# Optimization experiments

Hardware: AMD Instinct MI355X
Metric: run time of the kernel (lower is better)

Reference implementation:

```python
import jax, jax.numpy as jnp
import numpy as np

B, N, C = 16, 4096, 80
IOU_THR = 0.5
CONF_THR = 0.5
MAX_DET = 100
FROM_LOGITS = True


def setup_inputs() -> dict:
    key = jax.random.key(0)
    k1, k2 = jax.random.split(key)
    box_prediction = jax.random.uniform(k1, (B, N, 4), dtype=jnp.float32)
    class_prediction = jax.random.normal(k2, (B, N, C), dtype=jnp.float32)
    return {"box_prediction": box_prediction, "class_prediction": class_prediction}


def _pairwise_iou(b):
    # TF NMS kernel semantics: corners [y1,x1,y2,x2], normalized with min/max.
    y1 = jnp.minimum(b[:, 0], b[:, 2]); y2 = jnp.maximum(b[:, 0], b[:, 2])
    x1 = jnp.minimum(b[:, 1], b[:, 3]); x2 = jnp.maximum(b[:, 1], b[:, 3])
    area = (y2 - y1) * (x2 - x1)                      # [N]
    ih = jnp.maximum(0.0, jnp.minimum(y2[:, None], y2[None, :]) - jnp.maximum(y1[:, None], y1[None, :]))
    iw = jnp.maximum(0.0, jnp.minimum(x2[:, None], x2[None, :]) - jnp.maximum(x1[:, None], x1[None, :]))
    inter = ih * iw                                   # [N, N]
    union = area[:, None] + area[None, :] - inter
    return jnp.where(inter > 0.0, inter / union, 0.0)


def _nms_single(boxes, cls):
    # boxes [N,4], cls [N,C] -> padded ([MAX_DET,4], [MAX_DET,C])
    scores = jnp.max(cls, axis=1)                     # tf.reduce_max(cls_pred, axis=1)
    order = jnp.argsort(-scores)                      # descending, stable
    b = boxes[order]
    s = scores[order]
    valid = s > CONF_THR                              # score_threshold filter
    iou = _pairwise_iou(b)                            # [N, N]

    def body(keep, i):
        suppressed = jnp.any(keep & (iou[:, i] > IOU_THR))
        k = valid[i] & jnp.logical_not(suppressed)
        return keep.at[i].set(k), None

    keep, _ = jax.lax.scan(body, jnp.zeros(boxes.shape[0], dtype=bool), jnp.arange(boxes.shape[0]))
    # Compact kept boxes to the front (stable sort keeps descending-score order),
    # take the first MAX_DET slots, zero-pad the rest (fixed-shape analogue of
    # tf.image.non_max_suppression's variable-length index output).
    pos = jnp.argsort(jnp.logical_not(keep))[:MAX_DET]
    m = (jnp.arange(MAX_DET) < jnp.sum(keep))[:, None]
    out_idx = order[pos]
    nms_box = jnp.where(m, boxes[out_idx], 0.0)
    nms_cls = jnp.where(m, cls[out_idx], 0.0)
    return nms_box, nms_cls


def reference(box_prediction, class_prediction):
    # bounding_box_format == 'xywh' (absolute) -> convert_format is identity.
    if FROM_LOGITS:
        cls_predictions = jax.nn.softmax(jnp.square(class_prediction * 10.0), axis=-1)
    else:
        cls_predictions = class_prediction
    nms_box, nms_cls = jax.vmap(_nms_single)(box_prediction, cls_predictions)
    return nms_box, nms_cls, cls_predictions
```

## Files before the change

### kernel.cpp

```cpp
#include <hip/hip_runtime.h>
#include <cstdint>
#include <cstddef>

#define BB 16
#define NN 4096
#define CC 80
#define MAXD 100
#define CONF_T 0.5f
#define PER_B (MAXD * 4 + MAXD * CC)
#define NWORDS 64
#define FBCAP 2048
#define SEGSZ 2048

#define IOUC 0x1.000001p-1

#define WS_KEYS   0x000000
#define WS_NEED   0x200000

__global__ __launch_bounds__(256) void k_softmax(const float* __restrict__ cls_in,
                                                 float* __restrict__ probs,
                                                 uint64_t* __restrict__ keys) {
#pragma clang fp contract(off)
    int slot = blockIdx.x * 256 + threadIdx.x;
    int row  = slot >> 3;
    int j    = slot & 7;
    const float* rp = cls_in + (size_t)row * CC + j;

    float e[10];
    float m = -3.402823466e+38f;
    #pragma unroll
    for (int k = 0; k < 10; ++k) {
        float y = rp[8 * k] * 10.0f;
        float z = y * y;
        e[k] = z;
        m = fmaxf(m, z);
    }
    m = fmaxf(m, __shfl_xor(m, 1));
    m = fmaxf(m, __shfl_xor(m, 2));
    m = fmaxf(m, __shfl_xor(m, 4));

    #pragma unroll
    for (int k = 0; k < 10; ++k) e[k] = expf(e[k] - m);

    float acc = e[0];
    #pragma unroll
    for (int k = 1; k < 10; ++k) acc += e[k];
    acc = acc + __shfl_xor(acc, 1);
    acc = acc + __shfl_xor(acc, 2);
    acc = acc + __shfl_xor(acc, 4);

    float score = 1.0f / acc;
    float* pp = probs + (size_t)row * CC + j;
    #pragma unroll
    for (int k = 0; k < 10; ++k) pp[8 * k] = e[k] * score;

    if (j == 0) {
        unsigned n = (unsigned)(row & (NN - 1));
        keys[row] = ((uint64_t)__float_as_uint(score) << 32)
                  | (uint64_t)(0xFFFFFFFFu - n);
    }
}

__global__ __launch_bounds__(1024) void k_pnms(const uint64_t* __restrict__ keys,
                                               const float* __restrict__ boxes,
                                               const float* __restrict__ probs,
                                               float* __restrict__ out_box,
                                               float* __restrict__ out_cls) {
#pragma clang fp contract(off)
    __shared__ __align__(16) unsigned char sraw[6 * NN * 4];
    float* hy1 = (float*)sraw;
    float* hx1 = (float*)(sraw + NN * 4);
    float* hy2 = (float*)(sraw + 2 * NN * 4);
    float* hx2 = (float*)(sraw + 3 * NN * 4);
    float* har = (float*)(sraw + 4 * NN * 4);
    int*   og  = (int*)(sraw + 5 * NN * 4);
    uint64_t* bbuf = (uint64_t*)sraw;
    __shared__ uint64_t kill[64];
    __shared__ uint64_t persup[16];
    __shared__ float ky1[MAXD], kx1[MAXD], ky2[MAXD], kx2[MAXD], kar[MAXD];
    __shared__ int kpos[MAXD];
    __shared__ int fidx[MAXD];
    __shared__ int wsumA[16], wsumB[16];
    __shared__ int kept_s, done_s;

    const int tid = threadIdx.x, lane = tid & 63, wv = tid >> 6;
    const int b = blockIdx.x;
    const uint64_t* kb = keys + (size_t)b * NN;
    const float* bxp = boxes + (size_t)b * NN * 4;

    uint64_t myk[4]; bool fa[4], fb[4];
    int asum = 0, bsum = 0;
    for (int k = 0; k < 4; ++k) {
        uint64_t key = kb[4 * tid + k]; myk[k] = key;
        unsigned hi = (unsigned)(key >> 32);
        fa[k] = (hi == 0x3F800000u);
        fb[k] = (__uint_as_float(hi) > CONF_T) && !fa[k];
        asum += fa[k] ? 1 : 0; bsum += fb[k] ? 1 : 0;
    }
    int ia = asum, ib = bsum;
    for (int off = 1; off < 64; off <<= 1) {
        int va = __shfl_up(ia, off), vb = __shfl_up(ib, off);
        if (lane >= off) { ia += va; ib += vb; }
    }
    if (lane == 63) { wsumA[wv] = ia; wsumB[wv] = ib; }
    __syncthreads();
    int baseA = 0, baseB = 0, cntA = 0, cntB = 0;
    for (int w2 = 0; w2 < 16; ++w2) {
        if (w2 < wv) { baseA += wsumA[w2]; baseB += wsumB[w2]; }
        cntA += wsumA[w2]; cntB += wsumB[w2];
    }
    int pA = baseA + (ia - asum);
    int pB = baseB + (ib - bsum);
    for (int k = 0; k < 4; ++k) {
        if (fa[k]) og[pA++] = 4 * tid + k;
        if (fb[k]) bbuf[pB++] = myk[k];
    }
    __syncthreads();

    for (int i = tid; i < cntB; i += 1024) {
        uint64_t ki = bbuf[i];
        int rank = 0;
        for (int j = 0; j < cntB; ++j) rank += (bbuf[j] > ki) ? 1 : 0;
        og[cntA + rank] = (int)(0xFFFFFFFFu - (unsigned)(ki & 0xFFFFFFFFull));
    }
    int nl = cntA + cntB; if (nl > NN) nl = NN;
    __syncthreads();

    for (int i = tid; i < nl; i += 1024) {
        int o = og[i];
        float4 bv = ((const float4*)bxp)[o];
        float y1 = fminf(bv.x, bv.z), y2 = fmaxf(bv.x, bv.z);
        float x1 = fminf(bv.y, bv.w), x2 = fmaxf(bv.y, bv.w);
        hy1[i] = y1; hx1[i] = x1; hy2[i] = y2; hx2[i] = x2;
        har[i] = (y2 - y1) * (x2 - x1);
    }
    if (tid == 0) { kept_s = 0; done_s = 0; }

    int ng = (nl + 63) >> 6;
    for (int g = 0; g < ng; ++g) {
        __syncthreads();
        if (done_s) break;
        int kt = kept_s;
        int i = g * 64 + lane;
        bool v = i < nl;
        int ii = v ? i : 0;
        float y1 = hy1[ii], x1 = hx1[ii], y2 = hy2[ii], x2 = hx2[ii], ar = har[ii];

        bool killed = false;
        for (int q = wv; q < kt; q += 16) {
            float qy1 = ky1[q], qx1 = kx1[q], qy2 = ky2[q], qx2 = kx2[q], qar = kar[q];
            float ih = fmaxf(0.f, fminf(y2, qy2) - fmaxf(y1, qy1));
            float iw = fmaxf(0.f, fminf(x2, qx2) - fmaxf(x1, qx1));
            float inter = ih * iw;
            float uni = (ar + qar) - inter;
            killed = killed || (inter > 0.f && (double)inter > (double)uni * IOUC);
        }
        uint64_t pw = __ballot((!v) || killed);
        if (lane == 0) persup[wv] = pw;
        __syncthreads();
        uint64_t sup0 = 0;
        #pragma unroll
        for (int w2 = 0; w2 < 16; ++w2) sup0 |= persup[w2];
        if (sup0 == ~0ull) continue;

        #pragma unroll
        for (int r = 0; r < 4; ++r) {
            int t = wv + 16 * r;
            int it = g * 64 + t;
            bool tv = it < nl;
            int itx = tv ? it : 0;
            float ty1 = hy1[itx], tx1 = hx1[itx], ty2 = hy2[itx], tx2 = hx2[itx], tar = har[itx];
            float ih = fmaxf(0.f, fminf(ty2, y2) - fmaxf(ty1, y1));
            float iw = fmaxf(0.f, fminf(tx2, x2) - fmaxf(tx1, x1));
            float inter = ih * iw;
            float uni = (tar + ar) - inter;
            bool s = tv && v && (inter > 0.f) && ((double)inter > (double)uni * IOUC);
            uint64_t w = __ballot(s);
            if (lane == 0) kill[t] = w;
        }
        __syncthreads();

        if (wv == 0) {
            uint64_t sup = sup0, keptm = 0;
            #pragma unroll
            for (int c8 = 0; c8 < 8; ++c8) {
                uint64_t kk[8];
                #pragma unroll
                for (int u = 0; u < 8; ++u) kk[u] = kill[c8 * 8 + u];
                #pragma unroll
                for (int u = 0; u < 8; ++u) {
                    int t = c8 * 8 + u;
                    if (!((sup >> t) & 1ull)) { keptm |= 1ull << t; sup |= kk[u]; }
                }
            }
            int k0 = kept_s;
            if ((keptm >> lane) & 1ull) {
                int pos = k0 + __popcll(keptm & ((1ull << lane) - 1ull));
                if (pos < MAXD) {
                    kpos[pos] = i;
                    ky1[pos] = y1; kx1[pos] = x1;
                    ky2[pos] = y2; kx2[pos] = x2; kar[pos] = ar;
                }
            }
            if (lane == 0) {
                int k1 = k0 + __popcll(keptm);
                kept_s = k1;
                done_s = (k1 >= MAXD) ? 1 : 0;
            }
        }
    }
    __syncthreads();

    int kt = kept_s; if (kt > MAXD) kt = MAXD;
    if (tid < MAXD) fidx[tid] = (tid < kt) ? og[kpos[tid]] : 0;
    __syncthreads();

    float* ob = out_box + (size_t)b * MAXD * 4;
    float* oc = out_cls + (size_t)b * MAXD * CC;
    const float* pb = probs + (size_t)b * NN * CC;
    for (int r = tid; r < MAXD * 4; r += 1024) {
        int t = r >> 2, e2 = r & 3;
        float val = 0.0f;
        if (t < kt) { int idx = fidx[t]; val = bxp[(size_t)idx * 4 + e2]; }
        ob[r] = val;
    }
    for (int q = tid; q < MAXD * CC; q += 1024) {
        int t = q / CC, c = q - t * CC;
        float val = 0.0f;
        if (t < kt) { int idx = fidx[t]; val = pb[(size_t)idx * CC + c]; }
        oc[q] = val;
    }
}

__global__ __launch_bounds__(256) void k_gather(const float* __restrict__ boxes,
                                                const float* __restrict__ probs,
                                                const int* __restrict__ kidx,
                                                const int* __restrict__ cnt,
                                                float* __restrict__ out_box,
                                                float* __restrict__ out_cls) {
    int u = blockIdx.x * 256 + threadIdx.x;
    if (u >= BB * PER_B) return;
    int b = u / PER_B;
    int r = u - b * PER_B;
    int count = cnt[b];
    float val = 0.0f;
    if (r < MAXD * 4) {
        int t = r >> 2, e = r & 3;
        if (t < count) {
            int idx = kidx[b * MAXD + t];
            val = boxes[((size_t)b * NN + idx) * 4 + e];
        }
        out_box[(size_t)b * MAXD * 4 + r] = val;
    } else {
        int q = r - MAXD * 4;
        int t = q / CC, c = q - t * CC;
        if (t < count) {
            int idx = kidx[b * MAXD + t];
            val = probs[((size_t)b * NN + idx) * CC + c];
        }
        out_cls[(size_t)b * MAXD * CC + q] = val;
    }
}

__global__ __launch_bounds__(1024) void k_nms_fb(uint64_t* keys,
                                                 const float* __restrict__ boxes,
                                                 int* __restrict__ kidx_out,
                                                 int* __restrict__ cnt_out) {
#pragma clang fp contract(off)
    __shared__ float sy1[SEGSZ], sx1[SEGSZ], sy2[SEGSZ], sx2[SEGSZ];
    __shared__ int   soidx[SEGSZ];
    __shared__ uint64_t bbuf[FBCAP];
    __shared__ uint64_t sup[NWORDS];
    __shared__ float ky1[MAXD], kx1[MAXD], ky2[MAXD], kx2[MAXD], kar[MAXD];
    __shared__ int   keptidx[MAXD];
    __shared__ int   wsumA[16], wsumB[16];
    __shared__ int   keptcnt_s, ctrl_s, seg_s;

    const int tid = threadIdx.x, lane = tid & 63, wv = tid >> 6;
    const int b = blockIdx.x;
    const uint64_t* kb = keys + (size_t)b * NN;
    const float* bxp = boxes + (size_t)b * NN * 4;
    int* og = (int*)(keys + (size_t)b * NN);

    uint64_t myk[4]; bool fa[4], fb[4];
    int asum = 0, bsum = 0;
    for (int k = 0; k < 4; ++k) {
        uint64_t key = kb[4 * tid + k]; myk[k] = key;
        unsigned hi = (unsigned)(key >> 32);
        fa[k] = (hi == 0x3F800000u);
        fb[k] = (__uint_as_float(hi) > CONF_T) && !fa[k];
        asum += fa[k] ? 1 : 0; bsum += fb[k] ? 1 : 0;
    }
    int ia = asum, ib = bsum;
    for (int off = 1; off < 64; off <<= 1) {
        int va = __shfl_up(ia, off), vb = __shfl_up(ib, off);
        if (lane >= off) { ia += va; ib += vb; }
    }
    if (lane == 63) { wsumA[wv] = ia; wsumB[wv] = ib; }
    __syncthreads();
    int baseA = 0, baseB = 0, cntA = 0, cntB = 0;
    for (int w2 = 0; w2 < 16; ++w2) {
        if (w2 < wv) { baseA += wsumA[w2]; baseB += wsumB[w2]; }
        cntA += wsumA[w2]; cntB += wsumB[w2];
    }
    int pA = baseA + (ia - asum);
    int pB = baseB + (ib - bsum);
    for (int k = 0; k < 4; ++k) {
        if (fa[k]) og[pA++] = 4 * tid + k;
        if (fb[k]) { if (pB < FBCAP) bbuf[pB] = myk[k]; pB++; }
    }
    int cntBc = cntB < FBCAP ? cntB : FBCAP;
    int nlist = cntA + cntBc;
    if (tid == 0) { keptcnt_s = 0; seg_s = 0; }
    for (int i = tid; i < FBCAP; i += 1024) if (i >= cntB) bbuf[i] = 0;
    __syncthreads();

    for (unsigned k2 = 2; k2 <= FBCAP; k2 <<= 1) {
        for (unsigned j = k2 >> 1; j > 0; j >>= 1) {
            for (unsigned i = tid; i < FBCAP; i += 1024) {
                unsigned p = i ^ j;
                if (p > i) {
                    uint64_t va = bbuf[i], vb = bbuf[p];
                    bool desc = ((i & k2) == 0);
                    if (desc ? (va < vb) : (va > vb)) { bbuf[i] = vb; bbuf[p] = va; }
                }
            }
            __syncthreads();
        }
    }
    for (int i = tid; i < cntBc; i += 1024)
        og[cntA + i] = (int)(0xFFFFFFFFu - (unsigned)(bbuf[i] & 0xFFFFFFFFull));
    if (tid < NWORDS) {
        int lo = tid * 64;
        uint64_t mm;
        if (nlist <= lo) mm = ~0ull;
        else if (nlist >= lo + 64) mm = 0ull;
        else mm = (~0ull) << (nlist - lo);
        sup[tid] = mm;
    }
    __syncthreads();

    for (int i = tid; i < SEGSZ; i += 1024) {
        if (i < nlist) {
            int o = og[i];
            soidx[i] = o;
            const float* bp = bxp + (size_t)o * 4;
            float b0 = bp[0], b1 = bp[1], b2 = bp[2], b3 = bp[3];
            sy1[i] = fminf(b0, b2); sy2[i] = fmaxf(b0, b2);
            sx1[i] = fminf(b1, b3); sx2[i] = fmaxf(b1, b3);
        }
    }
    __syncthreads();

    int curw = 0, segr = 0;
    while (true) {
        if (tid == 0) {
            int code = -1;
            for (;;) {
                int wend = (segr + 1) * (SEGSZ / 64);
                if (curw >= wend) {
                    if (segr == 0 && nlist > SEGSZ) {
                        code = -2; segr = 1; seg_s = 1; curw = SEGSZ / 64;
                    } else code = -1;
                    break;
                }
                uint64_t live = ~sup[curw];
                if (live) {
                    int j = __ffsll((unsigned long long)live) - 1;
                    int sel = curw * 64 + j;
                    int li = sel - segr * SEGSZ;
                    int kc = keptcnt_s;
                    keptidx[kc] = soidx[li];
                    ky1[kc] = sy1[li]; kx1[kc] = sx1[li];
                    ky2[kc] = sy2[li]; kx2[kc] = sx2[li];
                    kar[kc] = (sy2[li] - sy1[li]) * (sx2[li] - sx1[li]);
                    keptcnt_s = kc + 1;
                    sup[curw] |= (1ull << j);
                    code = (kc + 1 >= MAXD) ? -1 : sel;
                    break;
                }
                ++curw;
            }
            ctrl_s = code;
        }
        __syncthreads();
        int c = ctrl_s;
        if (c == -1) break;

        if (c == -2) {
            for (int i = tid; i < SEGSZ; i += 1024) {
                int gi = SEGSZ + i;
                if (gi < nlist) {
                    int o = og[gi];
                    soidx[i] = o;
                    const float* bp = bxp + (size_t)o * 4;
                    float b0 = bp[0], b1 = bp[1], b2 = bp[2], b3 = bp[3];
                    sy1[i] = fminf(b0, b2); sy2[i] = fmaxf(b0, b2);
                    sx1[i] = fminf(b1, b3); sx2[i] = fmaxf(b1, b3);
                }
            }
            __syncthreads();
            int kc = keptcnt_s;
            for (int k = 0; k < 2; ++k) {
                int li = tid + k * 1024;
                float y1 = sy1[li], y2 = sy2[li], x1 = sx1[li], x2 = sx2[li];
                float ar = (y2 - y1) * (x2 - x1);
                bool s = false;
                for (int q = 0; q < kc; ++q) {
                    float ih = fmaxf(0.f, fminf(y2, ky2[q]) - fmaxf(y1, ky1[q]));
                    float iw = fmaxf(0.f, fminf(x2, kx2[q]) - fmaxf(x1, kx1[q]));
                    float inter = ih * iw;
                    float uni = (ar + kar[q]) - inter;
                    s = s || (inter > 0.f && inter / uni > 0.5f);
                }
                uint64_t bal = __ballot(s);
                if (lane == 0 && bal) {
                    int word = (SEGSZ + k * 1024 + wv * 64) >> 6;
                    sup[word] |= bal;
                }
            }
            __syncthreads();
            continue;
        }

        int sg = seg_s;
        int cl = c - sg * SEGSZ;
        float cy1 = sy1[cl], cy2 = sy2[cl], cx1 = sx1[cl], cx2 = sx2[cl];
        float car = (cy2 - cy1) * (cx2 - cx1);
        for (int k = 0; k < 2; ++k) {
            int li = tid + k * 1024;
            float y1 = sy1[li], y2 = sy2[li], x1 = sx1[li], x2 = sx2[li];
            float ar = (y2 - y1) * (x2 - x1);
            float ih = fmaxf(0.f, fminf(y2, cy2) - fmaxf(y1, cy1));
            float iw = fmaxf(0.f, fminf(x2, cx2) - fmaxf(x1, cx1));
            float inter = ih * iw;
            float uni = (ar + car) - inter;
            bool s = (inter > 0.f) && (inter / uni > 0.5f);
            uint64_t bal = __ballot(s);
            if (lane == 0 && bal) {
                int word = (sg * SEGSZ + k * 1024 + wv * 64) >> 6;
                sup[word] |= bal;
            }
        }
        __syncthreads();
    }

    if (tid == 0) cnt_out[b] = keptcnt_s;
    for (int i = tid; i < MAXD; i += 1024)
        kidx_out[b * MAXD + i] = (i < keptcnt_s) ? keptidx[i] : 0;
}

extern "C" void kernel_launch(void* const* d_in, const int* in_sizes, int n_in,
                              void* d_out, int out_size, void* d_ws, size_t ws_size,
                              hipStream_t stream) {
    const float* boxes = (const float*)d_in[0];
    const float* cls   = (const float*)d_in[1];
    float* out = (float*)d_out;
    float* out_box = out;
    float* out_cls = out + (size_t)BB * MAXD * 4;
    float* probs   = out + (size_t)BB * MAXD * 4 + (size_t)BB * MAXD * CC;

    char* ws = (char*)d_ws;
    uint64_t* keys = (uint64_t*)(ws + WS_KEYS);

    k_softmax<<<(BB * NN * 8) / 256, 256, 0, stream>>>(cls, probs, keys);

    if (ws_size >= (size_t)WS_NEED) {
        k_pnms<<<BB, 1024, 0, stream>>>(keys, boxes, probs, out_box, out_cls);
    } else {
        int* kidx = (int*)(ws + (size_t)BB * NN * sizeof(uint64_t));
        int* cnt  = kidx + BB * MAXD;
        k_nms_fb<<<BB, 1024, 0, stream>>>(keys, boxes, kidx, cnt);
        k_gather<<<(BB * PER_B + 255) / 256, 256, 0, stream>>>(boxes, probs, kidx, cnt,
                                                               out_box, out_cls);
    }
}
```

Before: 100.9 us.

## Fuse softmax producers and NMS consumers into one kernel with atomic handoff

Merges the softmax kernel and the per-batch NMS kernel into a single launch. The first 16 blocks do NMS and spin on per-batch atomic counters, while 512 producer blocks compute softmax and keys and then signal completion with release atomics. NMS blocks preload and normalize all boxes into shared memory while they wait, and index them through the sorted order instead of gathering after the sort. This removes a kernel launch boundary and overlaps the box loading with softmax, but it relies on the consumer blocks not starving the producers (a forward-progress assumption) and adds a memset launch.

New measurement: 134.4 us. 1.33x slower.

```diff
diff --git a/kernel.cpp b/kernel.cpp
--- a/kernel.cpp
+++ b/kernel.cpp
@@ -11,10 +11,14 @@
 #define NWORDS 64
 #define FBCAP 2048
 #define SEGSZ 2048
+#define PRODPB 32
+#define NMSB   BB
+#define NPROD  (BB * PRODPB)
 
 #define IOUC 0x1.000001p-1
 
 #define WS_KEYS   0x000000
+#define WS_CNT    0x100000
 #define WS_NEED   0x200000
 
 __global__ __launch_bounds__(256) void k_softmax(const float* __restrict__ cls_in,
@@ -61,32 +65,90 @@
     }
 }
 
-__global__ __launch_bounds__(1024) void k_pnms(const uint64_t* __restrict__ keys,
-                                               const float* __restrict__ boxes,
-                                               const float* __restrict__ probs,
-                                               float* __restrict__ out_box,
-                                               float* __restrict__ out_cls) {
+__global__ __launch_bounds__(1024) void k_fused(const float* __restrict__ boxes,
+                                                const float* __restrict__ cls_in,
+                                                float* __restrict__ probs,
+                                                uint64_t* __restrict__ keys,
+                                                int* cnt,
+                                                float* __restrict__ out_box,
+                                                float* __restrict__ out_cls) {
 #pragma clang fp contract(off)
-    __shared__ __align__(16) unsigned char sraw[6 * NN * 4];
-    float* hy1 = (float*)sraw;
-    float* hx1 = (float*)(sraw + NN * 4);
-    float* hy2 = (float*)(sraw + 2 * NN * 4);
-    float* hx2 = (float*)(sraw + 3 * NN * 4);
-    float* har = (float*)(sraw + 4 * NN * 4);
-    int*   og  = (int*)(sraw + 5 * NN * 4);
-    uint64_t* bbuf = (uint64_t*)sraw;
+    __shared__ float ry1[NN], rx1[NN], ry2[NN], rx2[NN], rar[NN];
+    __shared__ int og[NN];
+    __shared__ uint64_t bbuf[NN];
     __shared__ uint64_t kill[64];
     __shared__ uint64_t persup[16];
     __shared__ float ky1[MAXD], kx1[MAXD], ky2[MAXD], kx2[MAXD], kar[MAXD];
     __shared__ int kpos[MAXD];
-    __shared__ int fidx[MAXD];
     __shared__ int wsumA[16], wsumB[16];
     __shared__ int kept_s, done_s;
 
     const int tid = threadIdx.x, lane = tid & 63, wv = tid >> 6;
-    const int b = blockIdx.x;
+    const int blk = blockIdx.x;
+
+    if (blk >= NMSB) {
+        int p = blk - NMSB;
+        int batch = p >> 5;
+        int row = batch * NN + (p & 31) * 128 + (tid >> 3);
+        int j = tid & 7;
+        const float* rp = cls_in + (size_t)row * CC + j;
+
+        float e[10];
+        float m = -3.402823466e+38f;
+        #pragma unroll
+        for (int k = 0; k < 10; ++k) {
+            float y = rp[8 * k] * 10.0f;
+            float z = y * y;
+            e[k] = z;
+            m = fmaxf(m, z);
+        }
+        m = fmaxf(m, __shfl_xor(m, 1));
+        m = fmaxf(m, __shfl_xor(m, 2));
+        m = fmaxf(m, __shfl_xor(m, 4));
+        #pragma unroll
+        for (int k = 0; k < 10; ++k) e[k] = expf(e[k] - m);
+        float acc = e[0];
+        #pragma unroll
+        for (int k = 1; k < 10; ++k) acc += e[k];
+        acc = acc + __shfl_xor(acc, 1);
+        acc = acc + __shfl_xor(acc, 2);
+        acc = acc + __shfl_xor(acc, 4);
+        float score = 1.0f / acc;
+        float* pp = probs + (size_t)row * CC + j;
+        #pragma unroll
+        for (int k = 0; k < 10; ++k) pp[8 * k] = e[k] * score;
+        if (j == 0) {
+            unsigned n = (unsigned)(row & (NN - 1));
+            keys[row] = ((uint64_t)__float_as_uint(score) << 32)
+                      | (uint64_t)(0xFFFFFFFFu - n);
+        }
+        __syncthreads();
+        if (tid == 0) {
+            __threadfence();
+            __hip_atomic_fetch_add(&cnt[batch], 1, __ATOMIC_RELEASE,
+                                   __HIP_MEMORY_SCOPE_AGENT);
+        }
+        return;
+    }
+
+    const int b = blk;
+    const float* bxp = boxes + (size_t)b * NN * 4;
     const uint64_t* kb = keys + (size_t)b * NN;
-    const float* bxp = boxes + (size_t)b * NN * 4;
+
+    for (int i = tid; i < NN; i += 1024) {
+        float4 bv = ((const float4*)bxp)[i];
+        float y1 = fminf(bv.x, bv.z), y2 = fmaxf(bv.x, bv.z);
+        float x1 = fminf(bv.y, bv.w), x2 = fmaxf(bv.y, bv.w);
+        ry1[i] = y1; rx1[i] = x1; ry2[i] = y2; rx2[i] = x2;
+        rar[i] = (y2 - y1) * (x2 - x1);
+    }
+    if (tid == 0) {
+        while (__hip_atomic_load(&cnt[b], __ATOMIC_ACQUIRE,
+                                 __HIP_MEMORY_SCOPE_AGENT) < PRODPB)
+            __builtin_amdgcn_s_sleep(8);
+        __threadfence();
+    }
+    __syncthreads();
 
     uint64_t myk[4]; bool fa[4], fb[4];
     int asum = 0, bsum = 0;
@@ -124,16 +186,6 @@
         og[cntA + rank] = (int)(0xFFFFFFFFu - (unsigned)(ki & 0xFFFFFFFFull));
     }
     int nl = cntA + cntB; if (nl > NN) nl = NN;
-    __syncthreads();
-
-    for (int i = tid; i < nl; i += 1024) {
-        int o = og[i];
-        float4 bv = ((const float4*)bxp)[o];
-        float y1 = fminf(bv.x, bv.z), y2 = fmaxf(bv.x, bv.z);
-        float x1 = fminf(bv.y, bv.w), x2 = fmaxf(bv.y, bv.w);
-        hy1[i] = y1; hx1[i] = x1; hy2[i] = y2; hx2[i] = x2;
-        har[i] = (y2 - y1) * (x2 - x1);
-    }
     if (tid == 0) { kept_s = 0; done_s = 0; }
 
     int ng = (nl + 63) >> 6;
@@ -143,8 +195,8 @@
         int kt = kept_s;
         int i = g * 64 + lane;
         bool v = i < nl;
-        int ii = v ? i : 0;
-        float y1 = hy1[ii], x1 = hx1[ii], y2 = hy2[ii], x2 = hx2[ii], ar = har[ii];
+        int sog = v ? og[i] : 0;
+        float y1 = ry1[sog], x1 = rx1[sog], y2 = ry2[sog], x2 = rx2[sog], ar = rar[sog];
 
         bool killed = false;
         for (int q = wv; q < kt; q += 16) {
@@ -168,8 +220,8 @@
             int t = wv + 16 * r;
             int it = g * 64 + t;
             bool tv = it < nl;
-            int itx = tv ? it : 0;
-            float ty1 = hy1[itx], tx1 = hx1[itx], ty2 = hy2[itx], tx2 = hx2[itx], tar = har[itx];
+            int tog = tv ? og[it] : 0;
+            float ty1 = ry1[tog], tx1 = rx1[tog], ty2 = ry2[tog], tx2 = rx2[tog], tar = rar[tog];
             float ih = fmaxf(0.f, fminf(ty2, y2) - fmaxf(ty1, y1));
             float iw = fmaxf(0.f, fminf(tx2, x2) - fmaxf(tx1, x1));
             float inter = ih * iw;
@@ -197,7 +249,7 @@
             if ((keptm >> lane) & 1ull) {
                 int pos = k0 + __popcll(keptm & ((1ull << lane) - 1ull));
                 if (pos < MAXD) {
-                    kpos[pos] = i;
+                    kpos[pos] = sog;
                     ky1[pos] = y1; kx1[pos] = x1;
                     ky2[pos] = y2; kx2[pos] = x2; kar[pos] = ar;
                 }
@@ -211,23 +263,20 @@
     }
     __syncthreads();
 
-    int kt = kept_s; if (kt > MAXD) kt = MAXD;
-    if (tid < MAXD) fidx[tid] = (tid < kt) ? og[kpos[tid]] : 0;
-    __syncthreads();
-
+    int ktf = kept_s; if (ktf > MAXD) ktf = MAXD;
     float* ob = out_box + (size_t)b * MAXD * 4;
     float* oc = out_cls + (size_t)b * MAXD * CC;
     const float* pb = probs + (size_t)b * NN * CC;
     for (int r = tid; r < MAXD * 4; r += 1024) {
         int t = r >> 2, e2 = r & 3;
         float val = 0.0f;
-        if (t < kt) { int idx = fidx[t]; val = bxp[(size_t)idx * 4 + e2]; }
+        if (t < ktf) { int idx = kpos[t]; val = bxp[(size_t)idx * 4 + e2]; }
         ob[r] = val;
     }
     for (int q = tid; q < MAXD * CC; q += 1024) {
         int t = q / CC, c = q - t * CC;
         float val = 0.0f;
-        if (t < kt) { int idx = fidx[t]; val = pb[(size_t)idx * CC + c]; }
+        if (t < ktf) { int idx = kpos[t]; val = pb[(size_t)idx * CC + c]; }
         oc[q] = val;
     }
 }
@@ -463,11 +512,13 @@
     char* ws = (char*)d_ws;
     uint64_t* keys = (uint64_t*)(ws + WS_KEYS);
 
-    k_softmax<<<(BB * NN * 8) / 256, 256, 0, stream>>>(cls, probs, keys);
-
     if (ws_size >= (size_t)WS_NEED) {
-        k_pnms<<<BB, 1024, 0, stream>>>(keys, boxes, probs, out_box, out_cls);
+        int* cnt = (int*)(ws + WS_CNT);
+        hipMemsetAsync(cnt, 0, BB * sizeof(int), stream);
+        k_fused<<<NMSB + NPROD, 1024, 0, stream>>>(boxes, cls, probs, keys, cnt,
+                                                   out_box, out_cls);
     } else {
+        k_softmax<<<(BB * NN * 8) / 256, 256, 0, stream>>>(cls, probs, keys);
         int* kidx = (int*)(ws + (size_t)BB * NN * sizeof(uint64_t));
         int* cnt  = kidx + BB * MAXD;
         k_nms_fb<<<BB, 1024, 0, stream>>>(keys, boxes, kidx, cnt);
```

## Double-buffer intra-group kill masks and overlap next group's computation with serial resolve

Applied to the files above, without the earlier changes.

Precomputes the 64x64 intra-group suppression bitmasks for the next group while wave 0 runs the serial keep/suppress resolution for the current group, using a double-buffered kill array. This removes one block-wide barrier per group and hides the intra-group IoU work behind the serial scan. The cost is that fully suppressed groups still compute the next group's masks, and when a group is live only 15 waves share the prefetch work.

Measured after the change: 100.7 us. About the same (-0.2%).

```diff
diff --git a/kernel.cpp b/kernel.cpp
--- a/kernel.cpp
+++ b/kernel.cpp
@@ -75,7 +75,7 @@
     float* har = (float*)(sraw + 4 * NN * 4);
     int*   og  = (int*)(sraw + 5 * NN * 4);
     uint64_t* bbuf = (uint64_t*)sraw;
-    __shared__ uint64_t kill[64];
+    __shared__ uint64_t kill2[2][64];
     __shared__ uint64_t persup[16];
     __shared__ float ky1[MAXD], kx1[MAXD], ky2[MAXD], kx2[MAXD], kar[MAXD];
     __shared__ int kpos[MAXD];
@@ -135,11 +135,32 @@
         har[i] = (y2 - y1) * (x2 - x1);
     }
     if (tid == 0) { kept_s = 0; done_s = 0; }
+    __syncthreads();
 
     int ng = (nl + 63) >> 6;
+
+    if (ng > 0) {
+        int i2 = lane; bool v2 = i2 < nl; int ii2 = v2 ? i2 : 0;
+        float cy1 = hy1[ii2], cx1 = hx1[ii2], cy2 = hy2[ii2], cx2 = hx2[ii2], car = har[ii2];
+        #pragma unroll
+        for (int r = 0; r < 4; ++r) {
+            int t = wv + 16 * r;
+            bool tv = t < nl;
+            int itx = tv ? t : 0;
+            float ty1 = hy1[itx], tx1 = hx1[itx], ty2 = hy2[itx], tx2 = hx2[itx], tar = har[itx];
+            float ih = fmaxf(0.f, fminf(ty2, cy2) - fmaxf(ty1, cy1));
+            float iw = fmaxf(0.f, fminf(tx2, cx2) - fmaxf(tx1, cx1));
+            float inter = ih * iw;
+            float uni = (tar + car) - inter;
+            bool s = tv && v2 && (inter > 0.f) && ((double)inter > (double)uni * IOUC);
+            uint64_t w = __ballot(s);
+            if (lane == 0) kill2[0][t] = w;
+        }
+    }
+    __syncthreads();
+
+    int cur = 0;
     for (int g = 0; g < ng; ++g) {
-        __syncthreads();
-        if (done_s) break;
         int kt = kept_s;
         int i = g * 64 + lane;
         bool v = i < nl;
@@ -161,32 +182,18 @@
         uint64_t sup0 = 0;
         #pragma unroll
         for (int w2 = 0; w2 < 16; ++w2) sup0 |= persup[w2];
-        if (sup0 == ~0ull) continue;
-
-        #pragma unroll
-        for (int r = 0; r < 4; ++r) {
-            int t = wv + 16 * r;
-            int it = g * 64 + t;
-            bool tv = it < nl;
-            int itx = tv ? it : 0;
-            float ty1 = hy1[itx], tx1 = hx1[itx], ty2 = hy2[itx], tx2 = hx2[itx], tar = har[itx];
-            float ih = fmaxf(0.f, fminf(ty2, y2) - fmaxf(ty1, y1));
-            float iw = fmaxf(0.f, fminf(tx2, x2) - fmaxf(tx1, x1));
-            float inter = ih * iw;
-            float uni = (tar + ar) - inter;
-            bool s = tv && v && (inter > 0.f) && ((double)inter > (double)uni * IOUC);
-            uint64_t w = __ballot(s);
-            if (lane == 0) kill[t] = w;
-        }
-        __syncthreads();
-
-        if (wv == 0) {
+
+        int nxt = cur ^ 1;
+        bool live = (sup0 != ~0ull);
+        bool haveNext = (g + 1 < ng);
+
+        if (live && wv == 0) {
             uint64_t sup = sup0, keptm = 0;
             #pragma unroll
             for (int c8 = 0; c8 < 8; ++c8) {
                 uint64_t kk[8];
                 #pragma unroll
-                for (int u = 0; u < 8; ++u) kk[u] = kill[c8 * 8 + u];
+                for (int u = 0; u < 8; ++u) kk[u] = kill2[cur][c8 * 8 + u];
                 #pragma unroll
                 for (int u = 0; u < 8; ++u) {
                     int t = c8 * 8 + u;
@@ -207,7 +214,45 @@
                 kept_s = k1;
                 done_s = (k1 >= MAXD) ? 1 : 0;
             }
-        }
+        } else if (haveNext && (live ? (wv >= 1) : true)) {
+            int g2 = g + 1;
+            int i2 = g2 * 64 + lane; bool v2 = i2 < nl; int ii2 = v2 ? i2 : 0;
+            float cy1 = hy1[ii2], cx1 = hx1[ii2], cy2 = hy2[ii2], cx2 = hx2[ii2], car = har[ii2];
+            if (live) {
+                for (int t = wv - 1; t < 64; t += 15) {
+                    int it = g2 * 64 + t;
+                    bool tv = it < nl;
+                    int itx = tv ? it : 0;
+                    float ty1 = hy1[itx], tx1 = hx1[itx], ty2 = hy2[itx], tx2 = hx2[itx], tar = har[itx];
+                    float ih = fmaxf(0.f, fminf(ty2, cy2) - fmaxf(ty1, cy1));
+                    float iw = fmaxf(0.f, fminf(tx2, cx2) - fmaxf(tx1, cx1));
+                    float inter = ih * iw;
+                    float uni = (tar + car) - inter;
+                    bool s = tv && v2 && (inter > 0.f) && ((double)inter > (double)uni * IOUC);
+                    uint64_t w = __ballot(s);
+                    if (lane == 0) kill2[nxt][t] = w;
+                }
+            } else {
+                #pragma unroll
+                for (int r = 0; r < 4; ++r) {
+                    int t = wv + 16 * r;
+                    int it = g2 * 64 + t;
+                    bool tv = it < nl;
+                    int itx = tv ? it : 0;
+                    float ty1 = hy1[itx], tx1 = hx1[itx], ty2 = hy2[itx], tx2 = hx2[itx], tar = har[itx];
+                    float ih = fmaxf(0.f, fminf(ty2, cy2) - fmaxf(ty1, cy1));
+                    float iw = fmaxf(0.f, fminf(tx2, cx2) - fmaxf(tx1, cx1));
+                    float inter = ih * iw;
+                    float uni = (tar + car) - inter;
+                    bool s = tv && v2 && (inter > 0.f) && ((double)inter > (double)uni * IOUC);
+                    uint64_t w = __ballot(s);
+                    if (lane == 0) kill2[nxt][t] = w;
+                }
+            }
+        }
+        __syncthreads();
+        if (done_s) break;
+        cur = nxt;
     }
     __syncthreads();
 
```

## Process NMS candidates in 128-wide groups per iteration

Applied to the files above, without the earlier changes.

The greedy NMS loop now handles 128 candidates per group instead of 64. Each lane carries two candidate boxes and the intra-group kill matrix widens to 128x128 bits. This halves the number of group iterations and their block-wide barriers. The early skip for fully suppressed groups is removed, and the serial wave-0 resolve now does twice the work per group. Kept boxes may also overshoot the 100-detection limit by more candidates before the loop stops.

New measurement: 106.5 us. +5.6%, slower.

```diff
diff --git a/kernel.cpp b/kernel.cpp
--- a/kernel.cpp
+++ b/kernel.cpp
@@ -11,6 +11,7 @@
 #define NWORDS 64
 #define FBCAP 2048
 #define SEGSZ 2048
+#define TK 128
 
 #define IOUC 0x1.000001p-1
 
@@ -75,8 +76,8 @@
     float* har = (float*)(sraw + 4 * NN * 4);
     int*   og  = (int*)(sraw + 5 * NN * 4);
     uint64_t* bbuf = (uint64_t*)sraw;
-    __shared__ uint64_t kill[64];
-    __shared__ uint64_t persup[16];
+    __shared__ uint64_t kill[TK][2];
+    __shared__ uint64_t persup[16][2];
     __shared__ float ky1[MAXD], kx1[MAXD], ky2[MAXD], kx2[MAXD], kar[MAXD];
     __shared__ int kpos[MAXD];
     __shared__ int fidx[MAXD];
@@ -136,74 +137,109 @@
     }
     if (tid == 0) { kept_s = 0; done_s = 0; }
 
-    int ng = (nl + 63) >> 6;
+    int ng = (nl + TK - 1) / TK;
     for (int g = 0; g < ng; ++g) {
         __syncthreads();
         if (done_s) break;
         int kt = kept_s;
-        int i = g * 64 + lane;
-        bool v = i < nl;
-        int ii = v ? i : 0;
-        float y1 = hy1[ii], x1 = hx1[ii], y2 = hy2[ii], x2 = hx2[ii], ar = har[ii];
-
-        bool killed = false;
+        int i0 = g * TK + lane;
+        int i1 = i0 + 64;
+        bool v0 = i0 < nl, v1 = i1 < nl;
+        int ii0 = v0 ? i0 : 0, ii1 = v1 ? i1 : 0;
+        float a_y1 = hy1[ii0], a_x1 = hx1[ii0], a_y2 = hy2[ii0], a_x2 = hx2[ii0], a_ar = har[ii0];
+        float b_y1 = hy1[ii1], b_x1 = hx1[ii1], b_y2 = hy2[ii1], b_x2 = hx2[ii1], b_ar = har[ii1];
+
+        bool k0f = false, k1f = false;
         for (int q = wv; q < kt; q += 16) {
             float qy1 = ky1[q], qx1 = kx1[q], qy2 = ky2[q], qx2 = kx2[q], qar = kar[q];
-            float ih = fmaxf(0.f, fminf(y2, qy2) - fmaxf(y1, qy1));
-            float iw = fmaxf(0.f, fminf(x2, qx2) - fmaxf(x1, qx1));
-            float inter = ih * iw;
-            float uni = (ar + qar) - inter;
-            killed = killed || (inter > 0.f && (double)inter > (double)uni * IOUC);
-        }
-        uint64_t pw = __ballot((!v) || killed);
-        if (lane == 0) persup[wv] = pw;
-        __syncthreads();
-        uint64_t sup0 = 0;
+            float ih0 = fmaxf(0.f, fminf(a_y2, qy2) - fmaxf(a_y1, qy1));
+            float iw0 = fmaxf(0.f, fminf(a_x2, qx2) - fmaxf(a_x1, qx1));
+            float in0 = ih0 * iw0;
+            float un0 = (a_ar + qar) - in0;
+            k0f = k0f || (in0 > 0.f && (double)in0 > (double)un0 * IOUC);
+            float ih1 = fmaxf(0.f, fminf(b_y2, qy2) - fmaxf(b_y1, qy1));
+            float iw1 = fmaxf(0.f, fminf(b_x2, qx2) - fmaxf(b_x1, qx1));
+            float in1 = ih1 * iw1;
+            float un1 = (b_ar + qar) - in1;
+            k1f = k1f || (in1 > 0.f && (double)in1 > (double)un1 * IOUC);
+        }
+        uint64_t pw0 = __ballot((!v0) || k0f);
+        uint64_t pw1 = __ballot((!v1) || k1f);
+        if (lane == 0) { persup[wv][0] = pw0; persup[wv][1] = pw1; }
+
         #pragma unroll
-        for (int w2 = 0; w2 < 16; ++w2) sup0 |= persup[w2];
-        if (sup0 == ~0ull) continue;
-
-        #pragma unroll
-        for (int r = 0; r < 4; ++r) {
-            int t = wv + 16 * r;
-            int it = g * 64 + t;
+        for (int r = 0; r < 8; ++r) {
+            int t = wv * 8 + r;
+            int it = g * TK + t;
             bool tv = it < nl;
             int itx = tv ? it : 0;
             float ty1 = hy1[itx], tx1 = hx1[itx], ty2 = hy2[itx], tx2 = hx2[itx], tar = har[itx];
-            float ih = fmaxf(0.f, fminf(ty2, y2) - fmaxf(ty1, y1));
-            float iw = fmaxf(0.f, fminf(tx2, x2) - fmaxf(tx1, x1));
-            float inter = ih * iw;
-            float uni = (tar + ar) - inter;
-            bool s = tv && v && (inter > 0.f) && ((double)inter > (double)uni * IOUC);
-            uint64_t w = __ballot(s);
-            if (lane == 0) kill[t] = w;
+            float ih0 = fmaxf(0.f, fminf(ty2, a_y2) - fmaxf(ty1, a_y1));
+            float iw0 = fmaxf(0.f, fminf(tx2, a_x2) - fmaxf(tx1, a_x1));
+            float in0 = ih0 * iw0;
+            float un0 = (tar + a_ar) - in0;
+            bool s0 = tv && v0 && (in0 > 0.f) && ((double)in0 > (double)un0 * IOUC);
+            float ih1 = fmaxf(0.f, fminf(ty2, b_y2) - fmaxf(ty1, b_y1));
+            float iw1 = fmaxf(0.f, fminf(tx2, b_x2) - fmaxf(tx1, b_x1));
+            float in1 = ih1 * iw1;
+            float un1 = (tar + b_ar) - in1;
+            bool s1 = tv && v1 && (in1 > 0.f) && ((double)in1 > (double)un1 * IOUC);
+            uint64_t w0 = __ballot(s0);
+            uint64_t w1 = __ballot(s1);
+            if (lane == 0) { kill[t][0] = w0; kill[t][1] = w1; }
         }
         __syncthreads();
 
         if (wv == 0) {
-            uint64_t sup = sup0, keptm = 0;
+            uint64_t sup0 = 0, sup1 = 0;
+            #pragma unroll
+            for (int w2 = 0; w2 < 16; ++w2) { sup0 |= persup[w2][0]; sup1 |= persup[w2][1]; }
+            uint64_t m0 = 0, m1 = 0;
             #pragma unroll
             for (int c8 = 0; c8 < 8; ++c8) {
-                uint64_t kk[8];
+                uint64_t kk0[8], kk1[8];
                 #pragma unroll
-                for (int u = 0; u < 8; ++u) kk[u] = kill[c8 * 8 + u];
+                for (int u = 0; u < 8; ++u) { kk0[u] = kill[c8 * 8 + u][0]; kk1[u] = kill[c8 * 8 + u][1]; }
                 #pragma unroll
                 for (int u = 0; u < 8; ++u) {
                     int t = c8 * 8 + u;
-                    if (!((sup >> t) & 1ull)) { keptm |= 1ull << t; sup |= kk[u]; }
+                    if (!((sup0 >> t) & 1ull)) { m0 |= 1ull << t; sup0 |= kk0[u]; sup1 |= kk1[u]; }
+                }
+            }
+            #pragma unroll
+            for (int c8 = 0; c8 < 8; ++c8) {
+                uint64_t kk0[8], kk1[8];
+                #pragma unroll
+                for (int u = 0; u < 8; ++u) { kk0[u] = kill[64 + c8 * 8 + u][0]; kk1[u] = kill[64 + c8 * 8 + u][1]; }
+                #pragma unroll
+                for (int u = 0; u < 8; ++u) {
+                    int t = c8 * 8 + u;
+                    if (!((sup1 >> t) & 1ull)) { m1 |= 1ull << t; sup0 |= kk0[u]; sup1 |= kk1[u]; }
                 }
             }
             int k0 = kept_s;
-            if ((keptm >> lane) & 1ull) {
-                int pos = k0 + __popcll(keptm & ((1ull << lane) - 1ull));
+            int c0 = __popcll(m0), c1 = __popcll(m1);
+            uint64_t below = (1ull << lane) - 1ull;
+            if ((m0 >> lane) & 1ull) {
+                int pos = k0 + __popcll(m0 & below);
                 if (pos < MAXD) {
+                    int i = g * TK + lane;
                     kpos[pos] = i;
-                    ky1[pos] = y1; kx1[pos] = x1;
-                    ky2[pos] = y2; kx2[pos] = x2; kar[pos] = ar;
+                    ky1[pos] = hy1[i]; kx1[pos] = hx1[i];
+                    ky2[pos] = hy2[i]; kx2[pos] = hx2[i]; kar[pos] = har[i];
+                }
+            }
+            if ((m1 >> lane) & 1ull) {
+                int pos = k0 + c0 + __popcll(m1 & below);
+                if (pos < MAXD) {
+                    int i = g * TK + 64 + lane;
+                    kpos[pos] = i;
+                    ky1[pos] = hy1[i]; kx1[pos] = hx1[i];
+                    ky2[pos] = hy2[i]; kx2[pos] = hx2[i]; kar[pos] = har[i];
                 }
             }
             if (lane == 0) {
-                int k1 = k0 + __popcll(keptm);
+                int k1 = k0 + c0 + c1;
                 kept_s = k1;
                 done_s = (k1 >= MAXD) ? 1 : 0;
             }
```
